# Performance work log

Measured on AMD Instinct MI355X. Metric: run time of the kernel, lower is better.

The kernel has to match this reference:

```python
import jax, jax.numpy as jnp
import numpy as np

N = 50000          # num nodes
E_EDGES = 512000   # num edges
H = 64             # hidden_dim
HEADS = 4
DH = H // HEADS    # attn_dim = 16
CLAMP = 5.0
LN_EPS = 1e-5


def _layernorm(x, g, b):
    mu = x.mean(-1, keepdims=True)
    var = ((x - mu) ** 2).mean(-1, keepdims=True)
    return (x - mu) / jnp.sqrt(var + LN_EPS) * g + b


def setup_inputs() -> dict:
    key = jax.random.key(0)
    ks = jax.random.split(key, 16)
    f32 = jnp.float32
    def w(k, shp, scale=0.1):
        return jax.random.normal(k, shp, f32) * scale
    return {
        "x": jax.random.normal(ks[0], (N, H), f32),
        "e": jax.random.normal(ks[1], (E_EDGES, H), f32),
        "dst": jax.random.randint(ks[2], (E_EDGES,), 0, N),
        "src": jax.random.randint(ks[3], (E_EDGES,), 0, N),
        "qkv_w": w(ks[4], (3 * H, H)),
        "qkv_b": jnp.zeros((3 * H,), f32),
        "E_w": w(ks[5], (2 * H, H)),
        "E_b": jnp.zeros((2 * H,), f32),
        "Aw": w(ks[6], (DH, HEADS, 1)),
        "conn1_w": w(ks[7], (H, H)),
        "conn1_b": jnp.zeros((H,), f32),
        "conn2_w": w(ks[8], (H, H)),
        "conn2_b": jnp.zeros((H,), f32),
        "ffn1_w": w(ks[9], (2 * H, H)),
        "ffn1_b": jnp.zeros((2 * H,), f32),
        "ffn2_w": w(ks[10], (H, 2 * H)),
        "ffn2_b": jnp.zeros((H,), f32),
        "ln1h_g": jnp.ones((H,), f32), "ln1h_b": jnp.zeros((H,), f32),
        "ln2h_g": jnp.ones((H,), f32), "ln2h_b": jnp.zeros((H,), f32),
        "ln1c_g": jnp.ones((H,), f32), "ln1c_b": jnp.zeros((H,), f32),
        "ln2c_g": jnp.ones((H,), f32), "ln2c_b": jnp.zeros((H,), f32),
    }


def _forward(x, e, dst, src, qkv_w, qkv_b, E_w, E_b, Aw,
             conn1_w, conn1_b, conn2_w, conn2_b,
             ffn1_w, ffn1_b, ffn2_w, ffn2_b,
             ln1h_g, ln1h_b, ln2h_g, ln2h_b,
             ln1c_g, ln1c_b, ln2c_g, ln2c_b):
    n_nodes = x.shape[0]
    # packed QKV projection (torch Linear convention: x @ W.T + b)
    qkv = x @ qkv_w.T + qkv_b                       # [N, 3H]
    Qh, Kh, Vh = jnp.split(qkv, 3, axis=-1)         # each [N, H]
    Qdst, Ksrc, Vsrc = Qh[dst], Kh[src], Vh[src]    # [E, H]

    Eh = (e @ E_w.T + E_b).reshape(-1, 2, H)        # [E, 2, H]
    Ew, Eb = Eh[:, 0, :], Eh[:, 1, :]

    conn1 = (Qdst + Ksrc) * Ew                      # [E, H]
    # signed sqrt: sqrt(relu(x)) - sqrt(relu(-x)) == sign(x)*sqrt(|x|)
    conn2 = jnp.sign(conn1) * jnp.sqrt(jnp.abs(conn1))
    conn = jax.nn.relu(conn2 + Eb)                  # act = relu

    # edge score: einsum('ehd,dhc->ehc') with Aw [DH, HEADS, 1]
    conn_h = conn.reshape(-1, HEADS, DH)
    score = jnp.einsum('ehd,dhc->ehc', conn_h, Aw)  # [E, HEADS, 1]
    score = jnp.clip(score, -CLAMP, CLAMP)
    # pyg scatter softmax over dst groups
    smax = jax.ops.segment_max(score, dst, num_segments=n_nodes)
    sexp = jnp.exp(score - smax[dst])
    ssum = jax.ops.segment_sum(sexp, dst, num_segments=n_nodes)
    score = sexp / (ssum[dst] + 1e-16)

    conn = conn @ conn1_w.T + conn1_b               # conn_layer1
    msg = (Vsrc + conn).reshape(-1, HEADS, DH)
    agg = jax.ops.segment_sum(msg * score, dst, num_segments=n_nodes)
    agg = agg.reshape(n_nodes, H)

    h = x + agg
    h_res = h
    h = _layernorm(h, ln1h_g, ln1h_b)
    h = jax.nn.relu(h @ ffn1_w.T + ffn1_b) @ ffn2_w.T + ffn2_b
    h = _layernorm(h + h_res, ln2h_g, ln2h_b)

    conn = _layernorm(conn, ln1c_g, ln1c_b)
    conn = jax.nn.relu(conn)
    conn = conn @ conn2_w.T + conn2_b               # conn_layer2
    conn = _layernorm(conn + e, ln2c_g, ln2c_b)
    return h, conn


def reference(x, e, dst, src, qkv_w, qkv_b, E_w, E_b, Aw,
              conn1_w, conn1_b, conn2_w, conn2_b,
              ffn1_w, ffn1_b, ffn2_w, ffn2_b,
              ln1h_g, ln1h_b, ln2h_g, ln2h_b,
              ln1c_g, ln1c_b, ln2c_g, ln2c_b):
    return _forward(x, e, dst, src, qkv_w, qkv_b, E_w, E_b, Aw,
                    conn1_w, conn1_b, conn2_w, conn2_b,
                    ffn1_w, ffn1_b, ffn2_w, ffn2_b,
                    ln1h_g, ln1h_b, ln2h_g, ln2h_b,
                    ln1c_g, ln1c_b, ln2c_g, ln2c_b)
```

## Files before the change

### kernel.cpp

```cpp
#include <hip/hip_runtime.h>
#include <cstdint>

#define NN 50000
#define NE 512000

typedef unsigned short bf16u;
typedef __attribute__((ext_vector_type(8))) short short8v;
typedef __attribute__((ext_vector_type(4))) float f32x4;

__device__ __forceinline__ bf16u f2bf(float f){
  union { float f; unsigned int u; } v; v.f = f;
  unsigned int r = v.u + 0x7FFFu + ((v.u >> 16) & 1u);
  return (bf16u)(r >> 16);
}
__device__ __forceinline__ float bf2f(bf16u s){
  union { unsigned int u; float f; } v; v.u = ((unsigned int)s) << 16;
  return v.f;
}

__global__ void k0_pack(const float* __restrict__ E_w, const float* __restrict__ conn1_w,
                        const float* __restrict__ conn2_w, const float* __restrict__ qkv_w,
                        const float* __restrict__ ffn1_w, const float* __restrict__ ffn2_w,
                        const float* __restrict__ Aw,
                        bf16u* __restrict__ BpE, bf16u* __restrict__ Bp1,
                        bf16u* __restrict__ Bp2, bf16u* __restrict__ BpQ,
                        bf16u* __restrict__ BpF1, bf16u* __restrict__ BpF2,
                        bf16u* __restrict__ BpA){
  int i = blockIdx.x * 256 + threadIdx.x;
  int j = i & 7, l = (i >> 3) & 63;
  int nl = l & 15, kl = (l >> 4) << 3;
  if (i < 8192){
    int rest = i >> 9, nf = rest & 7, ks = rest >> 3;
    int n = nf * 16 + nl, k = ks * 32 + kl + j;
    BpE[i] = f2bf(E_w[n * 64 + k]);
  }
  if (i < 4096){
    int rest = i >> 9, nf = rest & 3, ks = rest >> 2;
    int n = nf * 16 + nl, k = ks * 32 + kl + j;
    Bp1[i] = f2bf(conn1_w[n * 64 + k]);
    Bp2[i] = f2bf(conn2_w[n * 64 + k]);
  }
  if (i < 12288){
    int rest = i >> 9, nf = rest % 12, ks = rest / 12;
    int n = nf * 16 + nl, k = ks * 32 + kl + j;
    BpQ[i] = f2bf(qkv_w[n * 64 + k]);
  }
  if (i < 8192){
    int rest = i >> 9, nf = rest & 7, ks = rest >> 3;
    int n = nf * 16 + nl, k = ks * 32 + kl + j;
    BpF1[i] = f2bf(ffn1_w[n * 64 + k]);
  }
  if (i < 8192){
    int rest = i >> 9, nf = rest & 3, ks = rest >> 2;
    int n = nf * 16 + nl, k = ks * 32 + kl + j;
    BpF2[i] = f2bf(ffn2_w[n * 128 + k]);
  }
  if (i < 1024){
    int ks = i >> 9;
    int n = nl, k = ks * 32 + kl + j;
    float v = (n < 4 && (k >> 4) == n) ? Aw[(k & 15) * 4 + n] : 0.f;
    BpA[i] = f2bf(v);
  }
}

__global__ void k_hist(const int* __restrict__ dst, int* __restrict__ cnt){
  int e = blockIdx.x * 256 + threadIdx.x;
  if (e < NE) atomicAdd(&cnt[dst[e]], 1);
}

#define SCAN_T 1024
#define PER_T 52
__global__ __launch_bounds__(SCAN_T) void k_scan(const int* __restrict__ cnt,
                                                 int* __restrict__ start, int* __restrict__ cursor){
  __shared__ int ls[SCAN_T];
  int t = threadIdx.x;
  int base = t * PER_T;
  int s = 0;
  const int4* cp = (const int4*)(cnt + base);
#pragma unroll
  for (int c = 0; c < 13; ++c){
    int4 v = cp[c];
    int n0 = base + c * 4;
    s += (n0 + 0 < NN ? v.x : 0) + (n0 + 1 < NN ? v.y : 0)
       + (n0 + 2 < NN ? v.z : 0) + (n0 + 3 < NN ? v.w : 0);
  }
  ls[t] = s; __syncthreads();
  for (int off = 1; off < SCAN_T; off <<= 1){
    int v = ls[t];
    int add = (t >= off) ? ls[t - off] : 0;
    __syncthreads();
    ls[t] = v + add;
    __syncthreads();
  }
  int run = (t > 0) ? ls[t - 1] : 0;
  for (int i = 0; i < PER_T; ++i){
    int n = base + i;
    if (n < NN){ start[n] = run; cursor[n] = run; run += cnt[n]; }
  }
  if (t == SCAN_T - 1) start[NN] = run;
}

__global__ void k_scatter(const int* __restrict__ dst, const int* __restrict__ src,
                          int* __restrict__ cursor, int4* __restrict__ pack){
  int e = blockIdx.x * 256 + threadIdx.x;
  if (e < NE){
    int dn = dst[e];
    int p = atomicAdd(&cursor[dn], 1);
    int4 rec; rec.x = e; rec.y = dn; rec.z = src[e]; rec.w = 0;
    pack[p] = rec;
  }
}

__global__ __launch_bounds__(256) void k1_qkv(const float* __restrict__ x,
    const bf16u* __restrict__ BpQ, const float* __restrict__ qkv_b,
    float* __restrict__ Q, float* __restrict__ K, float* __restrict__ V){
  int tile = blockIdx.x * 64;
  int w = threadIdx.x >> 6, l = threadIdx.x & 63;
  int lg = l >> 4, li = l & 15;
  const short8v* bpq = (const short8v*)BpQ;
  short8v Bq[3][2];
#pragma unroll
  for (int p = 0; p < 3; ++p)
#pragma unroll
    for (int ks = 0; ks < 2; ++ks)
      Bq[p][ks] = bpq[(ks * 12 + p * 4 + w) * 64 + l];
  f32x4 z = {0.f, 0.f, 0.f, 0.f};
  f32x4 acc[3][4];
#pragma unroll
  for (int p = 0; p < 3; ++p)
#pragma unroll
    for (int mf = 0; mf < 4; ++mf) acc[p][mf] = z;
#pragma unroll
  for (int mf = 0; mf < 4; ++mf){
    int row = tile + mf * 16 + li;
    bool g = row < NN;
    const float* xp = x + (size_t)row * 64 + lg * 8;
#pragma unroll
    for (int ks = 0; ks < 2; ++ks){
      float v[8];
      if (g){
        float4 t0 = *(const float4*)(xp + ks * 32);
        float4 t1 = *(const float4*)(xp + ks * 32 + 4);
        v[0]=t0.x; v[1]=t0.y; v[2]=t0.z; v[3]=t0.w;
        v[4]=t1.x; v[5]=t1.y; v[6]=t1.z; v[7]=t1.w;
      } else {
#pragma unroll
        for (int j = 0; j < 8; ++j) v[j] = 0.f;
      }
      short8v hi, lo;
#pragma unroll
      for (int j = 0; j < 8; ++j){
        bf16u h = f2bf(v[j]);
        hi[j] = (short)h;
        lo[j] = (short)f2bf(v[j] - bf2f(h));
      }
#pragma unroll
      for (int p = 0; p < 3; ++p){
        acc[p][mf] = __builtin_amdgcn_mfma_f32_16x16x32_bf16(hi, Bq[p][ks], acc[p][mf], 0, 0, 0);
        acc[p][mf] = __builtin_amdgcn_mfma_f32_16x16x32_bf16(lo, Bq[p][ks], acc[p][mf], 0, 0, 0);
      }
    }
  }
  float bias[3] = {qkv_b[w*16+li], qkv_b[64+w*16+li], qkv_b[128+w*16+li]};
  float* outs[3] = {Q, K, V};
#pragma unroll
  for (int p = 0; p < 3; ++p)
#pragma unroll
    for (int mf = 0; mf < 4; ++mf)
#pragma unroll
      for (int r = 0; r < 4; ++r){
        int row = tile + mf * 16 + lg * 4 + r;
        if (row < NN) outs[p][(size_t)row * 64 + w * 16 + li] = acc[p][mf][r] + bias[p];
      }
}

__global__ __launch_bounds__(256, 5) void k2_edge(
    const float* __restrict__ e, const int4* __restrict__ pack,
    const bf16u* __restrict__ BpE, const float* __restrict__ E_b,
    const bf16u* __restrict__ BpA, const bf16u* __restrict__ Bp1, const float* __restrict__ conn1_b,
    const float* __restrict__ Q, const float* __restrict__ K,
    const float* __restrict__ g1c, const float* __restrict__ b1c,
    const bf16u* __restrict__ Bp2, const float* __restrict__ conn2_b,
    const float* __restrict__ g2c, const float* __restrict__ b2c,
    bf16u* __restrict__ cm, float* __restrict__ sexp, float* __restrict__ out_conn){
  __shared__ bf16u ldsT[4 * 16 * 72];
  int t = threadIdx.x;
  int w = t >> 6, l = t & 63;
  int lg = l >> 4, li = l & 15;
  int pos0 = blockIdx.x * 64 + w * 16;
  bf16u* T = &ldsT[w * (16 * 72)];
  f32x4 z = {0.f, 0.f, 0.f, 0.f};

  short8v afr[2];
  {
    int eidA = pack[pos0 + li].x;
    const float* ep = e + (size_t)eidA * 64 + lg * 8;
#pragma unroll
    for (int ks = 0; ks < 2; ++ks){
      float4 a0 = *(const float4*)(ep + ks * 32);
      float4 a1 = *(const float4*)(ep + ks * 32 + 4);
      short8v af;
      af[0]=(short)f2bf(a0.x); af[1]=(short)f2bf(a0.y); af[2]=(short)f2bf(a0.z); af[3]=(short)f2bf(a0.w);
      af[4]=(short)f2bf(a1.x); af[5]=(short)f2bf(a1.y); af[6]=(short)f2bf(a1.z); af[7]=(short)f2bf(a1.w);
      afr[ks] = af;
    }
  }
  f32x4 accW[4], accB[4];
#pragma unroll
  for (int nf = 0; nf < 4; ++nf){ accW[nf] = z; accB[nf] = z; }
  {
    const short8v* bpe = (const short8v*)BpE;
#pragma unroll
    for (int ks = 0; ks < 2; ++ks){
#pragma unroll
      for (int nf = 0; nf < 4; ++nf){
        short8v BW = bpe[(ks * 8 + nf) * 64 + l];
        short8v BB = bpe[(ks * 8 + 4 + nf) * 64 + l];
        accW[nf] = __builtin_amdgcn_mfma_f32_16x16x32_bf16(afr[ks], BW, accW[nf], 0, 0, 0);
        accB[nf] = __builtin_amdgcn_mfma_f32_16x16x32_bf16(afr[ks], BB, accB[nf], 0, 0, 0);
      }
    }
  }

  int dnv[4], snv[4], eidv[4];
#pragma unroll
  for (int r = 0; r < 4; ++r){
    int4 rec = pack[pos0 + lg * 4 + r];
    eidv[r] = rec.x; dnv[r] = rec.y; snv[r] = rec.z;
  }
  float cp[4][4];
#pragma unroll
  for (int nf = 0; nf < 4; ++nf){
    int dim = nf * 16 + li;
    float eb0 = E_b[dim], eb1 = E_b[64 + dim];
#pragma unroll
    for (int r = 0; r < 4; ++r){
      float qv = Q[(size_t)dnv[r] * 64 + dim];
      float kv = K[(size_t)snv[r] * 64 + dim];
      float ew  = accW[nf][r] + eb0;
      float ebv = accB[nf][r] + eb1;
      float c1 = (qv + kv) * ew;
      float c2 = copysignf(sqrtf(fabsf(c1)), c1);
      cp[nf][r] = fmaxf(c2 + ebv, 0.f);
    }
  }

#pragma unroll
  for (int nf = 0; nf < 4; ++nf)
#pragma unroll
    for (int r = 0; r < 4; ++r)
      T[(lg * 4 + r) * 72 + nf * 16 + li] = f2bf(cp[nf][r]);
  __builtin_amdgcn_wave_barrier();
  short8v a1f[2];
  a1f[0] = *(const short8v*)&T[li * 72 + 0 * 32 + lg * 8];
  a1f[1] = *(const short8v*)&T[li * 72 + 1 * 32 + lg * 8];

  {
    const short8v* bpa = (const short8v*)BpA;
    f32x4 sacc = z;
    sacc = __builtin_amdgcn_mfma_f32_16x16x32_bf16(a1f[0], bpa[0 * 64 + l], sacc, 0, 0, 0);
    sacc = __builtin_amdgcn_mfma_f32_16x16x32_bf16(a1f[1], bpa[1 * 64 + l], sacc, 0, 0, 0);
    if (li < 4){
#pragma unroll
      for (int r = 0; r < 4; ++r){
        float sc = fminf(fmaxf(sacc[r], -5.f), 5.f);
        sexp[(size_t)(pos0 + lg * 4 + r) * 4 + li] = __expf(sc);
      }
    }
  }

  float cmv[4][4];
  {
    const short8v* bp1 = (const short8v*)Bp1;
#pragma unroll
    for (int nf = 0; nf < 4; ++nf){
      f32x4 acc = z;
      acc = __builtin_amdgcn_mfma_f32_16x16x32_bf16(a1f[0], bp1[(0 * 4 + nf) * 64 + l], acc, 0, 0, 0);
      acc = __builtin_amdgcn_mfma_f32_16x16x32_bf16(a1f[1], bp1[(1 * 4 + nf) * 64 + l], acc, 0, 0, 0);
      float c1b = conn1_b[nf * 16 + li];
#pragma unroll
      for (int r = 0; r < 4; ++r){
        float v = acc[r] + c1b;
        cmv[nf][r] = v;
        cm[(size_t)(pos0 + lg * 4 + r) * 64 + nf * 16 + li] = f2bf(v);
      }
    }
  }

  float mu1r[4], rs1r[4];
#pragma unroll
  for (int r = 0; r < 4; ++r){
    float s = cmv[0][r] + cmv[1][r] + cmv[2][r] + cmv[3][r];
    float q = cmv[0][r]*cmv[0][r] + cmv[1][r]*cmv[1][r] + cmv[2][r]*cmv[2][r] + cmv[3][r]*cmv[3][r];
    s += __shfl_xor(s, 1); s += __shfl_xor(s, 2); s += __shfl_xor(s, 4); s += __shfl_xor(s, 8);
    q += __shfl_xor(q, 1); q += __shfl_xor(q, 2); q += __shfl_xor(q, 4); q += __shfl_xor(q, 8);
    float mu = s * (1.f / 64.f);
    float var = q * (1.f / 64.f) - mu * mu;
    mu1r[r] = mu;
    rs1r[r] = rsqrtf(fmaxf(var, 0.f) + 1e-5f);
  }

  __builtin_amdgcn_wave_barrier();
#pragma unroll
  for (int nf = 0; nf < 4; ++nf){
    int dim = nf * 16 + li;
    float g1v = g1c[dim], b1v = b1c[dim];
#pragma unroll
    for (int r = 0; r < 4; ++r){
      float cn = fmaxf((cmv[nf][r] - mu1r[r]) * rs1r[r] * g1v + b1v, 0.f);
      T[(lg * 4 + r) * 72 + dim] = f2bf(cn);
    }
  }
  __builtin_amdgcn_wave_barrier();
  short8v a2f[2];
  a2f[0] = *(const short8v*)&T[li * 72 + 0 * 32 + lg * 8];
  a2f[1] = *(const short8v*)&T[li * 72 + 1 * 32 + lg * 8];

  float rv[4][4];
  {
    const short8v* bp2 = (const short8v*)Bp2;
#pragma unroll
    for (int nf = 0; nf < 4; ++nf){
      f32x4 acc = z;
      acc = __builtin_amdgcn_mfma_f32_16x16x32_bf16(a2f[0], bp2[(0 * 4 + nf) * 64 + l], acc, 0, 0, 0);
      acc = __builtin_amdgcn_mfma_f32_16x16x32_bf16(a2f[1], bp2[(1 * 4 + nf) * 64 + l], acc, 0, 0, 0);
      int dim = nf * 16 + li;
      float c2b = conn2_b[dim];
#pragma unroll
      for (int r = 0; r < 4; ++r)
        rv[nf][r] = acc[r] + c2b + e[(size_t)eidv[r] * 64 + dim];
    }
  }

#pragma unroll
  for (int r = 0; r < 4; ++r){
    float s = rv[0][r] + rv[1][r] + rv[2][r] + rv[3][r];
    float q = rv[0][r]*rv[0][r] + rv[1][r]*rv[1][r] + rv[2][r]*rv[2][r] + rv[3][r]*rv[3][r];
    s += __shfl_xor(s, 1); s += __shfl_xor(s, 2); s += __shfl_xor(s, 4); s += __shfl_xor(s, 8);
    q += __shfl_xor(q, 1); q += __shfl_xor(q, 2); q += __shfl_xor(q, 4); q += __shfl_xor(q, 8);
    float mu = s * (1.f / 64.f);
    float var = q * (1.f / 64.f) - mu * mu;
    float rs = rsqrtf(fmaxf(var, 0.f) + 1e-5f);
#pragma unroll
    for (int nf = 0; nf < 4; ++nf){
      int dim = nf * 16 + li;
      out_conn[(size_t)eidv[r] * 64 + dim] = (rv[nf][r] - mu) * rs * g2c[dim] + b2c[dim];
    }
  }
}

__global__ __launch_bounds__(256) void k_agg(
    const int* __restrict__ start, const int4* __restrict__ pack,
    const float* __restrict__ sexp, const bf16u* __restrict__ cm, const float* __restrict__ V,
    const float* __restrict__ x, float* __restrict__ hpre){
  int wid = (blockIdx.x * 256 + threadIdx.x) >> 6;
  int lane = threadIdx.x & 63;
  if (wid >= NN) return;
  int s0 = start[wid], s1 = start[wid + 1];
  int h = lane >> 4;
  float num0 = 0.f, den0 = 0.f, num1 = 0.f, den1 = 0.f;
  int i = s0;
  for (; i + 1 < s1; i += 2){
    float sxa = sexp[(size_t)i * 4 + h];
    float sxb = sexp[(size_t)(i + 1) * 4 + h];
    int sna = pack[i].z, snb = pack[i + 1].z;
    float va = V[(size_t)sna * 64 + lane];
    float vb = V[(size_t)snb * 64 + lane];
    float ca = bf2f(cm[(size_t)i * 64 + lane]);
    float cb = bf2f(cm[(size_t)(i + 1) * 64 + lane]);
    num0 += sxa * (va + ca); den0 += sxa;
    num1 += sxb * (vb + cb); den1 += sxb;
  }
  if (i < s1){
    float sx = sexp[(size_t)i * 4 + h];
    int sn = pack[i].z;
    float v  = V[(size_t)sn * 64 + lane];
    float cc = bf2f(cm[(size_t)i * 64 + lane]);
    num0 += sx * (v + cc); den0 += sx;
  }
  float num = num0 + num1, den = den0 + den1;
  hpre[(size_t)wid * 64 + lane] = x[(size_t)wid * 64 + lane] + num / (den + 1e-16f);
}

__global__ __launch_bounds__(256) void k5_node(
    const float* __restrict__ hpre,
    const float* __restrict__ g1, const float* __restrict__ b1,
    const bf16u* __restrict__ BpF1, const float* __restrict__ ffn1_b,
    const bf16u* __restrict__ BpF2, const float* __restrict__ ffn2_b,
    const float* __restrict__ g2, const float* __restrict__ b2,
    float* __restrict__ out_h){
  __shared__ bf16u hlhi[64 * 72];
  __shared__ bf16u hllo[64 * 72];
  __shared__ bf16u g1o[64 * 136];
  __shared__ float reds[64][4];
  __shared__ float redq[64][4];
  int tile = blockIdx.x * 64;
  int t = threadIdx.x;
  {
    int el = t >> 2, q = t & 3;
    int row = tile + el;
    bool g = row < NN;
    float v[16];
    if (g){
      const float4* hp = (const float4*)(hpre + (size_t)row * 64 + q * 16);
#pragma unroll
      for (int c = 0; c < 4; ++c){
        float4 tv = hp[c];
        v[c*4+0]=tv.x; v[c*4+1]=tv.y; v[c*4+2]=tv.z; v[c*4+3]=tv.w;
      }
    } else {
#pragma unroll
      for (int i = 0; i < 16; ++i) v[i] = 0.f;
    }
    float s = 0.f, sq = 0.f;
#pragma unroll
    for (int i = 0; i < 16; ++i){ s += v[i]; sq += v[i]*v[i]; }
    s  += __shfl_xor(s, 1);  s  += __shfl_xor(s, 2);
    sq += __shfl_xor(sq, 1); sq += __shfl_xor(sq, 2);
    float mu = s * (1.f/64.f);
    float var = sq * (1.f/64.f) - mu * mu;
    float rs = rsqrtf(fmaxf(var, 0.f) + 1e-5f);
#pragma unroll
    for (int i = 0; i < 16; ++i){
      int d = q * 16 + i;
      float hv = (v[i] - mu) * rs * g1[d] + b1[d];
      bf16u hb = f2bf(hv);
      hlhi[el * 72 + d] = hb;
      hllo[el * 72 + d] = f2bf(hv - bf2f(hb));
    }
  }
  __syncthreads();
  int w = t >> 6, l = t & 63;
  int lg = l >> 4, li = l & 15;
  const short8v* bpf1 = (const short8v*)BpF1;
  short8v B1f[2][2];
#pragma unroll
  for (int f = 0; f < 2; ++f)
#pragma unroll
    for (int ks = 0; ks < 2; ++ks)
      B1f[f][ks] = bpf1[(ks * 8 + f * 4 + w) * 64 + l];
  f32x4 z = {0.f, 0.f, 0.f, 0.f};
  f32x4 acc1[2][4];
#pragma unroll
  for (int f = 0; f < 2; ++f)
#pragma unroll
    for (int mf = 0; mf < 4; ++mf) acc1[f][mf] = z;
#pragma unroll
  for (int mf = 0; mf < 4; ++mf){
#pragma unroll
    for (int ks = 0; ks < 2; ++ks){
      const bf16u* ah = &hlhi[(mf * 16 + li) * 72 + ks * 32 + lg * 8];
      const bf16u* al = &hllo[(mf * 16 + li) * 72 + ks * 32 + lg * 8];
      short8v Ahi = *(const short8v*)ah;
      short8v Alo = *(const short8v*)al;
#pragma unroll
      for (int f = 0; f < 2; ++f){
        acc1[f][mf] = __builtin_amdgcn_mfma_f32_16x16x32_bf16(Ahi, B1f[f][ks], acc1[f][mf], 0, 0, 0);
        acc1[f][mf] = __builtin_amdgcn_mfma_f32_16x16x32_bf16(Alo, B1f[f][ks], acc1[f][mf], 0, 0, 0);
      }
    }
  }
  float fb[2] = {ffn1_b[w*16+li], ffn1_b[64+w*16+li]};
#pragma unroll
  for (int f = 0; f < 2; ++f)
#pragma unroll
    for (int mf = 0; mf < 4; ++mf)
#pragma unroll
      for (int r = 0; r < 4; ++r){
        int rowl = mf * 16 + lg * 4 + r;
        int col = f * 64 + w * 16 + li;
        g1o[rowl * 136 + col] = f2bf(fmaxf(acc1[f][mf][r] + fb[f], 0.f));
      }
  __syncthreads();
  const short8v* bpf2 = (const short8v*)BpF2;
  short8v B2f[4];
#pragma unroll
  for (int ks = 0; ks < 4; ++ks) B2f[ks] = bpf2[(ks * 4 + w) * 64 + l];
  int o = w * 16 + li;
  float f2b_ = ffn2_b[o];
  float racc[4][4];
#pragma unroll
  for (int mf = 0; mf < 4; ++mf){
    f32x4 acc = z;
#pragma unroll
    for (int ks = 0; ks < 4; ++ks){
      short8v A2 = *(const short8v*)&g1o[(mf * 16 + li) * 136 + ks * 32 + lg * 8];
      acc = __builtin_amdgcn_mfma_f32_16x16x32_bf16(A2, B2f[ks], acc, 0, 0, 0);
    }
#pragma unroll
    for (int r = 0; r < 4; ++r){
      int rowl = mf * 16 + lg * 4 + r;
      int row = tile + rowl;
      float hres = (row < NN) ? hpre[(size_t)row * 64 + o] : 0.f;
      float rvv = acc[r] + f2b_ + hres;
      racc[mf][r] = rvv;
      float s = rvv, q2 = rvv * rvv;
      s  += __shfl_xor(s, 1);  s  += __shfl_xor(s, 2);  s  += __shfl_xor(s, 4);  s  += __shfl_xor(s, 8);
      q2 += __shfl_xor(q2, 1); q2 += __shfl_xor(q2, 2); q2 += __shfl_xor(q2, 4); q2 += __shfl_xor(q2, 8);
      if (li == 0){ reds[rowl][w] = s; redq[rowl][w] = q2; }
    }
  }
  __syncthreads();
  float g2v = g2[o], b2v = b2[o];
#pragma unroll
  for (int mf = 0; mf < 4; ++mf){
#pragma unroll
    for (int r = 0; r < 4; ++r){
      int rowl = mf * 16 + lg * 4 + r;
      int row = tile + rowl;
      if (row < NN){
        float S  = reds[rowl][0] + reds[rowl][1] + reds[rowl][2] + reds[rowl][3];
        float Qq = redq[rowl][0] + redq[rowl][1] + redq[rowl][2] + redq[rowl][3];
        float mu2 = S * (1.f/64.f);
        float var2 = Qq * (1.f/64.f) - mu2 * mu2;
        float rs2 = rsqrtf(fmaxf(var2, 0.f) + 1e-5f);
        out_h[(size_t)row * 64 + o] = (racc[mf][r] - mu2) * rs2 * g2v + b2v;
      }
    }
  }
}

extern "C" void kernel_launch(void* const* d_in, const int* in_sizes, int n_in,
                              void* d_out, int out_size, void* d_ws, size_t ws_size,
                              hipStream_t stream){
  const float* x       = (const float*)d_in[0];
  const float* e       = (const float*)d_in[1];
  const int*   dst     = (const int*)d_in[2];
  const int*   src     = (const int*)d_in[3];
  const float* qkv_w   = (const float*)d_in[4];
  const float* qkv_b   = (const float*)d_in[5];
  const float* E_w     = (const float*)d_in[6];
  const float* E_b     = (const float*)d_in[7];
  const float* Aw      = (const float*)d_in[8];
  const float* conn1_w = (const float*)d_in[9];
  const float* conn1_b = (const float*)d_in[10];
  const float* conn2_w = (const float*)d_in[11];
  const float* conn2_b = (const float*)d_in[12];
  const float* ffn1_w  = (const float*)d_in[13];
  const float* ffn1_b  = (const float*)d_in[14];
  const float* ffn2_w  = (const float*)d_in[15];
  const float* ffn2_b  = (const float*)d_in[16];
  const float* ln1h_g  = (const float*)d_in[17];
  const float* ln1h_b  = (const float*)d_in[18];
  const float* ln2h_g  = (const float*)d_in[19];
  const float* ln2h_b  = (const float*)d_in[20];
  const float* ln1c_g  = (const float*)d_in[21];
  const float* ln1c_b  = (const float*)d_in[22];
  const float* ln2c_g  = (const float*)d_in[23];
  const float* ln2c_b  = (const float*)d_in[24];

  char* ws = (char*)d_ws;
  size_t off = 0;
  auto alloc = [&](size_t bytes) -> void* {
    void* p = ws + off;
    off += (bytes + 255) & ~(size_t)255;
    return p;
  };
  float* Q     = (float*)alloc((size_t)NN * 64 * 4);
  float* Kq    = (float*)alloc((size_t)NN * 64 * 4);
  float* V     = (float*)alloc((size_t)NN * 64 * 4);
  bf16u* cmb   = (bf16u*)alloc((size_t)NE * 64 * 2);
  float* sexp  = (float*)alloc((size_t)NE * 4 * 4);
  float* hpre  = (float*)alloc((size_t)NN * 64 * 4);
  bf16u* BpE   = (bf16u*)alloc(8192 * 2);
  bf16u* Bp1   = (bf16u*)alloc(4096 * 2);
  bf16u* Bp2   = (bf16u*)alloc(4096 * 2);
  bf16u* BpQ   = (bf16u*)alloc(12288 * 2);
  bf16u* BpF1  = (bf16u*)alloc(8192 * 2);
  bf16u* BpF2  = (bf16u*)alloc(8192 * 2);
  bf16u* BpA   = (bf16u*)alloc(1024 * 2);
  int*   cnt   = (int*)alloc((size_t)NN * 4);
  int*   startp= (int*)alloc(((size_t)NN + 1) * 4);
  int*   cursor= (int*)alloc((size_t)NN * 4);
  int4*  pack  = (int4*)alloc((size_t)NE * 16);

  float* out_h    = (float*)d_out;
  float* out_conn = out_h + (size_t)NN * 64;

  hipMemsetAsync(cnt, 0, (size_t)NN * 4, stream);

  k0_pack<<<48, 256, 0, stream>>>(E_w, conn1_w, conn2_w, qkv_w, ffn1_w, ffn2_w, Aw,
                                  BpE, Bp1, Bp2, BpQ, BpF1, BpF2, BpA);
  k_hist<<<NE / 256, 256, 0, stream>>>(dst, cnt);
  k_scan<<<1, SCAN_T, 0, stream>>>(cnt, startp, cursor);
  k_scatter<<<NE / 256, 256, 0, stream>>>(dst, src, cursor, pack);
  k1_qkv<<<(NN + 63) / 64, 256, 0, stream>>>(x, BpQ, qkv_b, Q, Kq, V);
  k2_edge<<<NE / 64, 256, 0, stream>>>(e, pack, BpE, E_b, BpA, Bp1, conn1_b,
                                       Q, Kq, ln1c_g, ln1c_b, Bp2, conn2_b,
                                       ln2c_g, ln2c_b, cmb, sexp, out_conn);
  k_agg<<<(NN * 64 + 255) / 256, 256, 0, stream>>>(startp, pack, sexp, cmb, V, x, hpre);
  k5_node<<<(NN + 63) / 64, 256, 0, stream>>>(hpre, ln1h_g, ln1h_b, BpF1, ffn1_b,
                                              BpF2, ffn2_b, ln2h_g, ln2h_b, out_h);
}
```

Baseline: 403.4 us.

## Fuse aggregation into node FFN kernel, split-bf16 conn MFMA, register-cached scan

Merges the per-node aggregation kernel into the node FFN/LayerNorm kernel. Each block's aggregated rows stay in shared memory, so the hpre buffer is never written to or read back from global memory, and one launch is removed. The scan kernel keeps its counts in registers instead of re-reading them from global memory. In the edge kernel, the conn activations are split into high and low bf16 parts and the MFMA count doubles, which raises accuracy at extra compute cost. The fused kernel gives each wave 16 nodes to aggregate serially, so parallelism for the gather drops from one wave per node to one wave per 16 nodes.

Result: faster. 392.5 us (-2.7%).

```diff
diff --git a/kernel.cpp b/kernel.cpp
--- a/kernel.cpp
+++ b/kernel.cpp
@@ -75,14 +75,19 @@
   __shared__ int ls[SCAN_T];
   int t = threadIdx.x;
   int base = t * PER_T;
+  int4 vs[13];
   int s = 0;
   const int4* cp = (const int4*)(cnt + base);
 #pragma unroll
   for (int c = 0; c < 13; ++c){
     int4 v = cp[c];
     int n0 = base + c * 4;
-    s += (n0 + 0 < NN ? v.x : 0) + (n0 + 1 < NN ? v.y : 0)
-       + (n0 + 2 < NN ? v.z : 0) + (n0 + 3 < NN ? v.w : 0);
+    if (n0 + 0 >= NN) v.x = 0;
+    if (n0 + 1 >= NN) v.y = 0;
+    if (n0 + 2 >= NN) v.z = 0;
+    if (n0 + 3 >= NN) v.w = 0;
+    vs[c] = v;
+    s += v.x + v.y + v.z + v.w;
   }
   ls[t] = s; __syncthreads();
   for (int off = 1; off < SCAN_T; off <<= 1){
@@ -93,9 +98,14 @@
     __syncthreads();
   }
   int run = (t > 0) ? ls[t - 1] : 0;
-  for (int i = 0; i < PER_T; ++i){
-    int n = base + i;
-    if (n < NN){ start[n] = run; cursor[n] = run; run += cnt[n]; }
+#pragma unroll
+  for (int c = 0; c < 13; ++c){
+    int vv[4] = {vs[c].x, vs[c].y, vs[c].z, vs[c].w};
+#pragma unroll
+    for (int j = 0; j < 4; ++j){
+      int n = base + c * 4 + j;
+      if (n < NN){ start[n] = run; cursor[n] = run; run += vv[j]; }
+    }
   }
   if (t == SCAN_T - 1) start[NN] = run;
 }
@@ -184,11 +194,13 @@
     const float* __restrict__ g2c, const float* __restrict__ b2c,
     bf16u* __restrict__ cm, float* __restrict__ sexp, float* __restrict__ out_conn){
   __shared__ bf16u ldsT[4 * 16 * 72];
+  __shared__ bf16u ldsTlo[4 * 16 * 72];
   int t = threadIdx.x;
   int w = t >> 6, l = t & 63;
   int lg = l >> 4, li = l & 15;
   int pos0 = blockIdx.x * 64 + w * 16;
-  bf16u* T = &ldsT[w * (16 * 72)];
+  bf16u* T   = &ldsT[w * (16 * 72)];
+  bf16u* Tlo = &ldsTlo[w * (16 * 72)];
   f32x4 z = {0.f, 0.f, 0.f, 0.f};
 
   short8v afr[2];
@@ -248,18 +260,26 @@
 #pragma unroll
   for (int nf = 0; nf < 4; ++nf)
 #pragma unroll
-    for (int r = 0; r < 4; ++r)
-      T[(lg * 4 + r) * 72 + nf * 16 + li] = f2bf(cp[nf][r]);
+    for (int r = 0; r < 4; ++r){
+      int idx = (lg * 4 + r) * 72 + nf * 16 + li;
+      bf16u hb = f2bf(cp[nf][r]);
+      T[idx] = hb;
+      Tlo[idx] = f2bf(cp[nf][r] - bf2f(hb));
+    }
   __builtin_amdgcn_wave_barrier();
-  short8v a1f[2];
-  a1f[0] = *(const short8v*)&T[li * 72 + 0 * 32 + lg * 8];
-  a1f[1] = *(const short8v*)&T[li * 72 + 1 * 32 + lg * 8];
+  short8v a1f[2], a1lo[2];
+  a1f[0]  = *(const short8v*)&T[li * 72 + 0 * 32 + lg * 8];
+  a1f[1]  = *(const short8v*)&T[li * 72 + 1 * 32 + lg * 8];
+  a1lo[0] = *(const short8v*)&Tlo[li * 72 + 0 * 32 + lg * 8];
+  a1lo[1] = *(const short8v*)&Tlo[li * 72 + 1 * 32 + lg * 8];
 
   {
     const short8v* bpa = (const short8v*)BpA;
     f32x4 sacc = z;
-    sacc = __builtin_amdgcn_mfma_f32_16x16x32_bf16(a1f[0], bpa[0 * 64 + l], sacc, 0, 0, 0);
-    sacc = __builtin_amdgcn_mfma_f32_16x16x32_bf16(a1f[1], bpa[1 * 64 + l], sacc, 0, 0, 0);
+    sacc = __builtin_amdgcn_mfma_f32_16x16x32_bf16(a1f[0],  bpa[0 * 64 + l], sacc, 0, 0, 0);
+    sacc = __builtin_amdgcn_mfma_f32_16x16x32_bf16(a1lo[0], bpa[0 * 64 + l], sacc, 0, 0, 0);
+    sacc = __builtin_amdgcn_mfma_f32_16x16x32_bf16(a1f[1],  bpa[1 * 64 + l], sacc, 0, 0, 0);
+    sacc = __builtin_amdgcn_mfma_f32_16x16x32_bf16(a1lo[1], bpa[1 * 64 + l], sacc, 0, 0, 0);
     if (li < 4){
 #pragma unroll
       for (int r = 0; r < 4; ++r){
@@ -275,8 +295,10 @@
 #pragma unroll
     for (int nf = 0; nf < 4; ++nf){
       f32x4 acc = z;
-      acc = __builtin_amdgcn_mfma_f32_16x16x32_bf16(a1f[0], bp1[(0 * 4 + nf) * 64 + l], acc, 0, 0, 0);
-      acc = __builtin_amdgcn_mfma_f32_16x16x32_bf16(a1f[1], bp1[(1 * 4 + nf) * 64 + l], acc, 0, 0, 0);
+      acc = __builtin_amdgcn_mfma_f32_16x16x32_bf16(a1f[0],  bp1[(0 * 4 + nf) * 64 + l], acc, 0, 0, 0);
+      acc = __builtin_amdgcn_mfma_f32_16x16x32_bf16(a1lo[0], bp1[(0 * 4 + nf) * 64 + l], acc, 0, 0, 0);
+      acc = __builtin_amdgcn_mfma_f32_16x16x32_bf16(a1f[1],  bp1[(1 * 4 + nf) * 64 + l], acc, 0, 0, 0);
+      acc = __builtin_amdgcn_mfma_f32_16x16x32_bf16(a1lo[1], bp1[(1 * 4 + nf) * 64 + l], acc, 0, 0, 0);
       float c1b = conn1_b[nf * 16 + li];
 #pragma unroll
       for (int r = 0; r < 4; ++r){
@@ -349,68 +371,67 @@
   }
 }
 
-__global__ __launch_bounds__(256) void k_agg(
+__global__ __launch_bounds__(256) void k_agg5(
     const int* __restrict__ start, const int4* __restrict__ pack,
     const float* __restrict__ sexp, const bf16u* __restrict__ cm, const float* __restrict__ V,
-    const float* __restrict__ x, float* __restrict__ hpre){
-  int wid = (blockIdx.x * 256 + threadIdx.x) >> 6;
-  int lane = threadIdx.x & 63;
-  if (wid >= NN) return;
-  int s0 = start[wid], s1 = start[wid + 1];
-  int h = lane >> 4;
-  float num0 = 0.f, den0 = 0.f, num1 = 0.f, den1 = 0.f;
-  int i = s0;
-  for (; i + 1 < s1; i += 2){
-    float sxa = sexp[(size_t)i * 4 + h];
-    float sxb = sexp[(size_t)(i + 1) * 4 + h];
-    int sna = pack[i].z, snb = pack[i + 1].z;
-    float va = V[(size_t)sna * 64 + lane];
-    float vb = V[(size_t)snb * 64 + lane];
-    float ca = bf2f(cm[(size_t)i * 64 + lane]);
-    float cb = bf2f(cm[(size_t)(i + 1) * 64 + lane]);
-    num0 += sxa * (va + ca); den0 += sxa;
-    num1 += sxb * (vb + cb); den1 += sxb;
-  }
-  if (i < s1){
-    float sx = sexp[(size_t)i * 4 + h];
-    int sn = pack[i].z;
-    float v  = V[(size_t)sn * 64 + lane];
-    float cc = bf2f(cm[(size_t)i * 64 + lane]);
-    num0 += sx * (v + cc); den0 += sx;
-  }
-  float num = num0 + num1, den = den0 + den1;
-  hpre[(size_t)wid * 64 + lane] = x[(size_t)wid * 64 + lane] + num / (den + 1e-16f);
-}
-
-__global__ __launch_bounds__(256) void k5_node(
-    const float* __restrict__ hpre,
+    const float* __restrict__ x,
     const float* __restrict__ g1, const float* __restrict__ b1,
     const bf16u* __restrict__ BpF1, const float* __restrict__ ffn1_b,
     const bf16u* __restrict__ BpF2, const float* __restrict__ ffn2_b,
     const float* __restrict__ g2, const float* __restrict__ b2,
     float* __restrict__ out_h){
-  __shared__ bf16u hlhi[64 * 72];
-  __shared__ bf16u hllo[64 * 72];
-  __shared__ bf16u g1o[64 * 136];
+  __shared__ float hpreS[64 * 68];
+  __shared__ bf16u buf1[64 * 72 * 2];
   __shared__ float reds[64][4];
   __shared__ float redq[64][4];
+  bf16u* hlhi = buf1;
+  bf16u* hllo = buf1 + 64 * 72;
+  bf16u* g1o  = buf1;
   int tile = blockIdx.x * 64;
   int t = threadIdx.x;
+  int w = t >> 6, l = t & 63;
+  int lg = l >> 4, li = l & 15;
+
+  for (int nl = w * 16; nl < w * 16 + 16; ++nl){
+    int node = tile + nl;
+    float hp = 0.f;
+    if (node < NN){
+      int s0 = start[node], s1 = start[node + 1];
+      int h = l >> 4;
+      float num0 = 0.f, den0 = 0.f, num1 = 0.f, den1 = 0.f;
+      int i = s0;
+      for (; i + 1 < s1; i += 2){
+        float sxa = sexp[(size_t)i * 4 + h];
+        float sxb = sexp[(size_t)(i + 1) * 4 + h];
+        int sna = pack[i].z, snb = pack[i + 1].z;
+        float va = V[(size_t)sna * 64 + l];
+        float vb = V[(size_t)snb * 64 + l];
+        float ca = bf2f(cm[(size_t)i * 64 + l]);
+        float cb = bf2f(cm[(size_t)(i + 1) * 64 + l]);
+        num0 += sxa * (va + ca); den0 += sxa;
+        num1 += sxb * (vb + cb); den1 += sxb;
+      }
+      if (i < s1){
+        float sx = sexp[(size_t)i * 4 + h];
+        int sn = pack[i].z;
+        float v  = V[(size_t)sn * 64 + l];
+        float cc = bf2f(cm[(size_t)i * 64 + l]);
+        num0 += sx * (v + cc); den0 += sx;
+      }
+      hp = x[(size_t)node * 64 + l] + (num0 + num1) / (den0 + den1 + 1e-16f);
+    }
+    hpreS[nl * 68 + l] = hp;
+  }
+  __syncthreads();
+
   {
     int el = t >> 2, q = t & 3;
-    int row = tile + el;
-    bool g = row < NN;
+    const float4* hp = (const float4*)&hpreS[el * 68 + q * 16];
     float v[16];
-    if (g){
-      const float4* hp = (const float4*)(hpre + (size_t)row * 64 + q * 16);
-#pragma unroll
-      for (int c = 0; c < 4; ++c){
-        float4 tv = hp[c];
-        v[c*4+0]=tv.x; v[c*4+1]=tv.y; v[c*4+2]=tv.z; v[c*4+3]=tv.w;
-      }
-    } else {
-#pragma unroll
-      for (int i = 0; i < 16; ++i) v[i] = 0.f;
+#pragma unroll
+    for (int c = 0; c < 4; ++c){
+      float4 tv = hp[c];
+      v[c*4+0]=tv.x; v[c*4+1]=tv.y; v[c*4+2]=tv.z; v[c*4+3]=tv.w;
     }
     float s = 0.f, sq = 0.f;
 #pragma unroll
@@ -430,8 +451,7 @@
     }
   }
   __syncthreads();
-  int w = t >> 6, l = t & 63;
-  int lg = l >> 4, li = l & 15;
+
   const short8v* bpf1 = (const short8v*)BpF1;
   short8v B1f[2][2];
 #pragma unroll
@@ -460,6 +480,7 @@
       }
     }
   }
+  __syncthreads();
   float fb[2] = {ffn1_b[w*16+li], ffn1_b[64+w*16+li]};
 #pragma unroll
   for (int f = 0; f < 2; ++f)
@@ -472,6 +493,7 @@
         g1o[rowl * 136 + col] = f2bf(fmaxf(acc1[f][mf][r] + fb[f], 0.f));
       }
   __syncthreads();
+
   const short8v* bpf2 = (const short8v*)BpF2;
   short8v B2f[4];
 #pragma unroll
@@ -490,8 +512,7 @@
 #pragma unroll
     for (int r = 0; r < 4; ++r){
       int rowl = mf * 16 + lg * 4 + r;
-      int row = tile + rowl;
-      float hres = (row < NN) ? hpre[(size_t)row * 64 + o] : 0.f;
+      float hres = hpreS[rowl * 68 + o];
       float rvv = acc[r] + f2b_ + hres;
       racc[mf][r] = rvv;
       float s = rvv, q2 = rvv * rvv;
@@ -561,7 +582,6 @@
   float* V     = (float*)alloc((size_t)NN * 64 * 4);
   bf16u* cmb   = (bf16u*)alloc((size_t)NE * 64 * 2);
   float* sexp  = (float*)alloc((size_t)NE * 4 * 4);
-  float* hpre  = (float*)alloc((size_t)NN * 64 * 4);
   bf16u* BpE   = (bf16u*)alloc(8192 * 2);
   bf16u* Bp1   = (bf16u*)alloc(4096 * 2);
   bf16u* Bp2   = (bf16u*)alloc(4096 * 2);
@@ -588,7 +608,7 @@
   k2_edge<<<NE / 64, 256, 0, stream>>>(e, pack, BpE, E_b, BpA, Bp1, conn1_b,
                                        Q, Kq, ln1c_g, ln1c_b, Bp2, conn2_b,
                                        ln2c_g, ln2c_b, cmb, sexp, out_conn);
-  k_agg<<<(NN * 64 + 255) / 256, 256, 0, stream>>>(startp, pack, sexp, cmb, V, x, hpre);
-  k5_node<<<(NN + 63) / 64, 256, 0, stream>>>(hpre, ln1h_g, ln1h_b, BpF1, ffn1_b,
-                                              BpF2, ffn2_b, ln2h_g, ln2h_b, out_h);
-}
+  k_agg5<<<(NN + 63) / 64, 256, 0, stream>>>(startp, pack, sexp, cmb, V, x,
+                                             ln1h_g, ln1h_b, BpF1, ffn1_b,
+                                             BpF2, ffn2_b, ln2h_g, ln2h_b, out_h);
+}
```
